# Kernel tuning notes

Hardware: AMD Instinct MI355X
Metric: run time of the kernel (lower is better)

## Reference

```python
import jax, jax.numpy as jnp
import numpy as np
from jax import lax

D_MODEL = 512
N_STATE = 64
L = 1024
NC = 4  # n_components
HIDDEN = 2 * D_MODEL  # ChannelMix mult=2
R = D_MODEL // 8      # SE reduction
EPS = 1e-5


def hippo_A(N):
    n = np.arange(N, dtype=np.float32)
    t = 2.0 * n + 1.0
    sq = np.sqrt(t[:, None] * t[None, :])
    A = -np.tril(sq, -1) - np.diag(n + 1.0)
    return jnp.asarray(A, jnp.float32)


def setup_inputs() -> dict:
    key = jax.random.key(0)
    ks = jax.random.split(key, 12)
    d, N = D_MODEL, N_STATE
    n = np.arange(N, dtype=np.float32)
    Bref = jnp.asarray(np.sqrt(2.0 * n + 1.0), jnp.float32)
    Bp = jnp.tile(Bref[None, None, :], (NC, d, 1)) + 0.01 * jax.random.normal(ks[0], (NC, d, N))
    Cp = 0.1 * jax.random.normal(ks[1], (NC, d, N))
    Dp = jnp.zeros((NC, d))
    log_dt = jnp.log(0.1 * (1.5 ** jnp.arange(NC, dtype=jnp.float32)))
    x = jax.random.normal(ks[2], (8, L, d))
    s = 0.02
    return {
        "x": x,
        "Bp": Bp, "Cp": Cp, "Dp": Dp, "log_dt": log_dt,
        "se_w1": s * jax.random.normal(ks[3], (R, d)), "se_b1": jnp.zeros((R,)),
        "se_w2": s * jax.random.normal(ks[4], (d, R)), "se_b2": jnp.zeros((d,)),
        "n1_g": jnp.ones((d,)), "n1_b": jnp.zeros((d,)),
        "up_w": s * jax.random.normal(ks[5], (2 * HIDDEN, d)), "up_b": jnp.zeros((2 * HIDDEN,)),
        "down_w": s * jax.random.normal(ks[6], (d, HIDDEN)), "down_b": jnp.zeros((d,)),
        "mixn_g": jnp.ones((d,)), "mixn_b": jnp.zeros((d,)),
        "n2_g": jnp.ones((d,)), "n2_b": jnp.zeros((d,)),
    }


def _ln(x, g, b):
    m = jnp.mean(x, axis=-1, keepdims=True)
    v = jnp.mean(jnp.square(x - m), axis=-1, keepdims=True)
    return (x - m) * lax.rsqrt(v + EPS) * g + b


def _mixture_kernel(Bp, Cp, Dp, log_dt):
    A = hippo_A(N_STATE)
    I = jnp.eye(N_STATE, dtype=jnp.float32)

    def one(Bc, Cc, Dc, ldt):
        dt = jax.nn.softplus(ldt) + 1e-6
        lhs = I - 0.5 * dt * A
        rhs = I + 0.5 * dt * A
        A_bar = jnp.linalg.solve(lhs, rhs)          # (N,N)
        B_bar = jnp.linalg.solve(lhs, (dt * Bc).T).T  # (d,N)

        def step(xs, _):
            y = jnp.einsum('dn,dn->d', Cc, xs)
            return xs @ A_bar.T, y

        _, ys = lax.scan(step, B_bar, None, length=L)  # (L,d)
        K = ys.T  # (d,L)
        return K.at[:, 0].add(Dc)

    return jax.vmap(one)(Bp, Cp, Dp, log_dt).sum(0)  # (d,L)


def reference(x, Bp, Cp, Dp, log_dt,
              se_w1, se_b1, se_w2, se_b2,
              n1_g, n1_b, up_w, up_b, down_w, down_b,
              mixn_g, mixn_b, n2_g, n2_b):
    d = D_MODEL
    K = _mixture_kernel(Bp, Cp, Dp, log_dt)  # (d,L)

    # causal full-length depthwise conv1d
    x_dw = jnp.transpose(x, (0, 2, 1))  # (B,C,T)
    x_pad = jnp.pad(x_dw, ((0, 0), (0, 0), (L - 1, 0)))
    y = lax.conv_general_dilated(
        x_pad, K[:, None, :], window_strides=(1,), padding='VALID',
        feature_group_count=d, dimension_numbers=('NCH', 'OIH', 'NCH'))
    y = jnp.transpose(y, (0, 2, 1))  # (B,T,C)

    # SE gate (squeeze over time)
    s = jnp.mean(y, axis=1)  # (B,C)
    h = jax.nn.relu(s @ se_w1.T + se_b1)
    g = jax.nn.sigmoid(h @ se_w2.T + se_b2)
    y = y * g[:, None, :]

    y1 = _ln(x + y, n1_g, n1_b)

    # ChannelMix (GLU MLP) with residual + LN
    u = y1 @ up_w.T + up_b
    a, gg = jnp.split(u, 2, axis=-1)
    z = (jax.nn.gelu(a, approximate=False) * jax.nn.sigmoid(gg)) @ down_w.T + down_b
    z = _ln(y1 + z, mixn_g, mixn_b)

    return _ln(y1 + z, n2_g, n2_b)
```

## Files before the change

### kernel.cpp

```cpp
#include <hip/hip_runtime.h>
#include <math.h>


typedef short bf16x8 __attribute__((ext_vector_type(8)));
typedef float f32x4 __attribute__((ext_vector_type(4)));

__device__ __forceinline__ float sigmoidf_(float x) { return 1.0f / (1.0f + expf(-x)); }
__device__ __forceinline__ float fast_sigmoid(float x) { return 1.0f / (1.0f + __expf(-x)); }
__device__ __forceinline__ float fast_gelu(float x) {
    float u = 0.7978845608f * (x + 0.044715f * x * x * x);
    float t = 1.0f - 2.0f / (1.0f + __expf(2.0f * u));
    return 0.5f * x * (1.0f + t);
}
__device__ __forceinline__ unsigned short f2bf(float f) {
    unsigned u = __float_as_uint(f);
    unsigned r = (u + 0x7FFFu + ((u >> 16) & 1u)) >> 16;
    return (unsigned short)r;
}
__device__ __forceinline__ unsigned pk2(unsigned short a, unsigned short b) {
    return (unsigned)a | ((unsigned)b << 16);
}
__device__ __forceinline__ void gload16(const void* g, void* l) {
    __builtin_amdgcn_global_load_lds((const __attribute__((address_space(1))) unsigned int*)g,
                                     (__attribute__((address_space(3))) unsigned int*)l, 16, 0, 0);
}

__global__ __launch_bounds__(256) void prep_comp(const float* __restrict__ log_dt,
                                                 float* __restrict__ Pow,
                                                 float* __restrict__ dtbuf) {
    int comp = blockIdx.x, tid = threadIdx.x;
    __shared__ __align__(16) float M1[4096];
    __shared__ __align__(16) float M1T[4096];
    __shared__ __align__(16) float M2[4096];
    __shared__ __align__(16) float M2T[4096];
    float ldt = log_dt[comp];
    float dt = log1pf(expf(ldt)) + 1e-6f;
    float hdt = 0.5f * dt;
    if (tid < 64) {
        int j = tid;
        float sqj = sqrtf(2.0f * (float)j + 1.0f);
        float S = 0.0f;
        for (int i = 0; i < 64; ++i) {
            float sqi = sqrtf(2.0f * (float)i + 1.0f);
            float r = (i == j) ? (1.0f - hdt * (float)(i + 1))
                               : ((i > j) ? (-hdt * sqi * sqj) : 0.0f);
            float X = (r - hdt * sqi * S) / (1.0f + hdt * (float)(i + 1));
            M1[i * 64 + j] = X;
            M1T[j * 64 + i] = X;
            S += sqi * X;
        }
    }
    __syncthreads();
    for (int ii = tid; ii < 4096; ii += 256) Pow[(size_t)comp * 40960 + ii] = M1[ii];
    float* cur = M1; float* curT = M1T; float* nxt = M2; float* nxtT = M2T;
    int ti = tid >> 4, tj = tid & 15;
    for (int s = 1; s <= 9; ++s) {
        float c[4][4] = {{0}};
#pragma unroll 8
        for (int k = 0; k < 64; ++k) {
            float4 a = *(const float4*)&curT[k * 64 + ti * 4];
            float4 b = *(const float4*)&cur[k * 64 + tj * 4];
            c[0][0] += a.x * b.x; c[0][1] += a.x * b.y; c[0][2] += a.x * b.z; c[0][3] += a.x * b.w;
            c[1][0] += a.y * b.x; c[1][1] += a.y * b.y; c[1][2] += a.y * b.z; c[1][3] += a.y * b.w;
            c[2][0] += a.z * b.x; c[2][1] += a.z * b.y; c[2][2] += a.z * b.z; c[2][3] += a.z * b.w;
            c[3][0] += a.w * b.x; c[3][1] += a.w * b.y; c[3][2] += a.w * b.z; c[3][3] += a.w * b.w;
        }
#pragma unroll
        for (int r = 0; r < 4; ++r) {
            float4 row; row.x = c[r][0]; row.y = c[r][1]; row.z = c[r][2]; row.w = c[r][3];
            *(float4*)&nxt[(ti * 4 + r) * 64 + tj * 4] = row;
            float4 colv; colv.x = c[0][r]; colv.y = c[1][r]; colv.z = c[2][r]; colv.w = c[3][r];
            *(float4*)&nxtT[(tj * 4 + r) * 64 + ti * 4] = colv;
        }
        __syncthreads();
        for (int ii = tid; ii < 4096; ii += 256) Pow[(size_t)comp * 40960 + s * 4096 + ii] = nxt[ii];
        float* t0 = cur; cur = nxt; nxt = t0;
        float* t1 = curT; curT = nxtT; nxtT = t1;
        __syncthreads();
    }
    if (tid == 0) dtbuf[comp] = dt;
}

__global__ __launch_bounds__(256) void compute_bbar(const float* __restrict__ Bp,
                                                    const float* __restrict__ dtbuf,
                                                    unsigned short* __restrict__ Bb_h,
                                                    unsigned short* __restrict__ Bb_l) {
    int gid = blockIdx.x * 256 + threadIdx.x;
    int comp = gid >> 9;
    float dt = dtbuf[comp];
    float hdt = 0.5f * dt;
    const float* bp = Bp + (size_t)gid * 64;
    unsigned short* oh = Bb_h + (size_t)gid * 64;
    unsigned short* ol = Bb_l + (size_t)gid * 64;
    float S = 0.0f;
    for (int i = 0; i < 64; ++i) {
        float sqi = sqrtf(2.0f * (float)i + 1.0f);
        float y = (dt * bp[i] - hdt * sqi * S) / (1.0f + hdt * (float)(i + 1));
        unsigned short h = f2bf(y);
        oh[i] = h;
        ol[i] = f2bf(y - __uint_as_float((unsigned)h << 16));
        S += sqi * y;
    }
}

__global__ __launch_bounds__(256) void convert_all(const float* __restrict__ up_w,
                                                   const float* __restrict__ dn_w,
                                                   const float* __restrict__ Cp,
                                                   unsigned short* __restrict__ up_wb,
                                                   unsigned short* __restrict__ dn_wb,
                                                   unsigned short* __restrict__ Cp_h,
                                                   unsigned short* __restrict__ Cp_l) {
    int i = blockIdx.x * 256 + threadIdx.x;
    if (i < 196608) {
        const float* src = (i < 131072) ? up_w : dn_w;
        unsigned short* dst = (i < 131072) ? up_wb : dn_wb;
        int j = (i < 131072) ? i : (i - 131072);
        float4 a = ((const float4*)src)[2 * j];
        float4 b = ((const float4*)src)[2 * j + 1];
        uint4 o;
        o.x = pk2(f2bf(a.x), f2bf(a.y));
        o.y = pk2(f2bf(a.z), f2bf(a.w));
        o.z = pk2(f2bf(b.x), f2bf(b.y));
        o.w = pk2(f2bf(b.z), f2bf(b.w));
        *(uint4*)&dst[(size_t)j * 8] = o;
    } else if (i < 212992) {
        int j = i - 196608;
        float4 a = ((const float4*)Cp)[2 * j];
        float4 b = ((const float4*)Cp)[2 * j + 1];
        float vv[8] = {a.x, a.y, a.z, a.w, b.x, b.y, b.z, b.w};
        unsigned short hs[8], ls[8];
#pragma unroll
        for (int k = 0; k < 8; ++k) {
            unsigned short h = f2bf(vv[k]);
            hs[k] = h;
            ls[k] = f2bf(vv[k] - __uint_as_float((unsigned)h << 16));
        }
        uint4 ho, lo;
        ho.x = pk2(hs[0], hs[1]); ho.y = pk2(hs[2], hs[3]); ho.z = pk2(hs[4], hs[5]); ho.w = pk2(hs[6], hs[7]);
        lo.x = pk2(ls[0], ls[1]); lo.y = pk2(ls[2], ls[3]); lo.z = pk2(ls[4], ls[5]); lo.w = pk2(ls[6], ls[7]);
        *(uint4*)&Cp_h[(size_t)j * 8] = ho;
        *(uint4*)&Cp_l[(size_t)j * 8] = lo;
    }
}

__global__ __launch_bounds__(256) void power_mats(const float* __restrict__ Pow,
                                                  unsigned short* __restrict__ Pst_h,
                                                  unsigned short* __restrict__ Pst_l,
                                                  unsigned short* __restrict__ Qst_h,
                                                  unsigned short* __restrict__ Qst_l) {
    int idx = blockIdx.x, comp = blockIdx.y, tid = threadIdx.x;
    __shared__ __align__(16) float R[4096], RT[4096], R2[4096], R2T[4096], SbT[4096];
    int isP = (idx < 32) ? 1 : 0;
    int f = isP ? idx : (idx - 32);
    int base_s = isP ? 0 : 5;
    const float* PowC = Pow + (size_t)comp * 40960;
    int i_ = tid & 63, kc = (tid >> 6) * 16;
    float* cur = R; float* curT = RT; float* nx = R2; float* nxT = R2T;
    if (f == 0) {
        for (int ii = tid; ii < 4096; ii += 256) {
            float v = ((ii >> 6) == (ii & 63)) ? 1.0f : 0.0f;
            R[ii] = v; RT[ii] = v;
        }
        __syncthreads();
    } else {
        int b0 = __ffs(f) - 1;
        const float* S0 = PowC + (size_t)(base_s + b0) * 4096;
#pragma unroll
        for (int j = 0; j < 16; j += 4) {
            float4 v = *(const float4*)&S0[i_ * 64 + kc + j];
            *(float4*)&R[i_ * 64 + kc + j] = v;
            RT[(kc + j + 0) * 64 + i_] = v.x;
            RT[(kc + j + 1) * 64 + i_] = v.y;
            RT[(kc + j + 2) * 64 + i_] = v.z;
            RT[(kc + j + 3) * 64 + i_] = v.w;
        }
        int rem = f & ~(1 << b0);
        int ti = tid >> 4, tj = tid & 15;
        __syncthreads();
        while (rem) {
            int b = __ffs(rem) - 1; rem &= rem - 1;
            const float* Sb = PowC + (size_t)(base_s + b) * 4096;
#pragma unroll
            for (int j = 0; j < 16; j += 4) {
                float4 v = *(const float4*)&Sb[i_ * 64 + kc + j];
                SbT[(kc + j + 0) * 64 + i_] = v.x;
                SbT[(kc + j + 1) * 64 + i_] = v.y;
                SbT[(kc + j + 2) * 64 + i_] = v.z;
                SbT[(kc + j + 3) * 64 + i_] = v.w;
            }
            __syncthreads();
            float c[4][4] = {{0}};
#pragma unroll 8
            for (int k = 0; k < 64; ++k) {
                float4 a = *(const float4*)&SbT[k * 64 + ti * 4];
                float4 b4 = *(const float4*)&cur[k * 64 + tj * 4];
                c[0][0] += a.x * b4.x; c[0][1] += a.x * b4.y; c[0][2] += a.x * b4.z; c[0][3] += a.x * b4.w;
                c[1][0] += a.y * b4.x; c[1][1] += a.y * b4.y; c[1][2] += a.y * b4.z; c[1][3] += a.y * b4.w;
                c[2][0] += a.z * b4.x; c[2][1] += a.z * b4.y; c[2][2] += a.z * b4.z; c[2][3] += a.z * b4.w;
                c[3][0] += a.w * b4.x; c[3][1] += a.w * b4.y; c[3][2] += a.w * b4.z; c[3][3] += a.w * b4.w;
            }
#pragma unroll
            for (int r = 0; r < 4; ++r) {
                float4 row; row.x = c[r][0]; row.y = c[r][1]; row.z = c[r][2]; row.w = c[r][3];
                *(float4*)&nx[(ti * 4 + r) * 64 + tj * 4] = row;
                float4 colv; colv.x = c[0][r]; colv.y = c[1][r]; colv.z = c[2][r]; colv.w = c[3][r];
                *(float4*)&nxT[(tj * 4 + r) * 64 + ti * 4] = colv;
            }
            __syncthreads();
            float* t0 = cur; cur = nx; nx = t0;
            float* t1 = curT; curT = nxT; nxT = t1;
        }
    }
    const float* src = isP ? cur : curT;
    int outrow = isP ? idx : (idx - 32);
    unsigned short* dh = (isP ? Pst_h : Qst_h) + (size_t)comp * 131072 + (size_t)outrow * 4096;
    unsigned short* dl = (isP ? Pst_l : Qst_l) + (size_t)comp * 131072 + (size_t)outrow * 4096;
    for (int ii = tid * 8; ii < 4096; ii += 2048) {
        float4 v0 = *(const float4*)&src[ii];
        float4 v1 = *(const float4*)&src[ii + 4];
        float vv[8] = {v0.x, v0.y, v0.z, v0.w, v1.x, v1.y, v1.z, v1.w};
        unsigned short hs[8], ls[8];
#pragma unroll
        for (int j = 0; j < 8; ++j) {
            unsigned short h = f2bf(vv[j]);
            hs[j] = h;
            ls[j] = f2bf(vv[j] - __uint_as_float((unsigned)h << 16));
        }
        uint4 ho, lo;
        ho.x = pk2(hs[0], hs[1]); ho.y = pk2(hs[2], hs[3]); ho.z = pk2(hs[4], hs[5]); ho.w = pk2(hs[6], hs[7]);
        lo.x = pk2(ls[0], ls[1]); lo.y = pk2(ls[2], ls[3]); lo.z = pk2(ls[4], ls[5]); lo.w = pk2(ls[6], ls[7]);
        *(uint4*)&dh[ii] = ho;
        *(uint4*)&dl[ii] = lo;
    }
}

__global__ __launch_bounds__(256) void kgemm_uv2(const unsigned short* __restrict__ Bb_h,
                                                 const unsigned short* __restrict__ Bb_l,
                                                 const unsigned short* __restrict__ Pst_h,
                                                 const unsigned short* __restrict__ Pst_l,
                                                 const unsigned short* __restrict__ Cp_h,
                                                 const unsigned short* __restrict__ Cp_l,
                                                 const unsigned short* __restrict__ Qst_h,
                                                 const unsigned short* __restrict__ Qst_l,
                                                 unsigned short* __restrict__ V_h,
                                                 unsigned short* __restrict__ V_l,
                                                 unsigned short* __restrict__ U_h,
                                                 unsigned short* __restrict__ U_l) {
    int zz = blockIdx.z;
    int isV = (zz < 4) ? 1 : 0;
    int comp = isV ? zz : (zz - 4);
    const unsigned short* Ah = isV ? Bb_h : Cp_h;
    const unsigned short* Al = isV ? Bb_l : Cp_l;
    const unsigned short* Bh = isV ? Pst_h : Qst_h;
    const unsigned short* Bl = isV ? Pst_l : Qst_l;
    unsigned short* Ch = isV ? V_h : U_h;
    unsigned short* Cl = isV ? V_l : U_l;
    int m0 = blockIdx.x * 128, n0 = blockIdx.y * 64;
    int tid = threadIdx.x, w = tid >> 6, l = tid & 63;
    __shared__ __align__(16) short Ash[8192], Asl[8192], Bsh[4096], Bsl[4096];
    const unsigned short* Abh = Ah + (size_t)comp * 32768;
    const unsigned short* Abl = Al + (size_t)comp * 32768;
    const unsigned short* Bbh = Bh + (size_t)comp * 131072;
    const unsigned short* Bbl = Bl + (size_t)comp * 131072;
#pragma unroll
    for (int i = 0; i < 4; ++i) {
        int cid = tid + 256 * i;
        int row = cid >> 3, slot = cid & 7;
        int goff = (m0 + row) * 64 + slot * 8;
        int loff = row * 64 + (slot ^ (row & 7)) * 8;
        *(uint4*)&Ash[loff] = *(const uint4*)(Abh + goff);
        *(uint4*)&Asl[loff] = *(const uint4*)(Abl + goff);
    }
#pragma unroll
    for (int i = 0; i < 2; ++i) {
        int cid = tid + 256 * i;
        int row = cid >> 3, slot = cid & 7;
        int goff = (n0 + row) * 64 + slot * 8;
        int loff = row * 64 + (slot ^ (row & 7)) * 8;
        *(uint4*)&Bsh[loff] = *(const uint4*)(Bbh + goff);
        *(uint4*)&Bsl[loff] = *(const uint4*)(Bbl + goff);
    }
    __syncthreads();
    int p = l >> 4, lr = l & 15;
    f32x4 acc[2][4];
#pragma unroll
    for (int rt = 0; rt < 2; ++rt)
#pragma unroll
        for (int ct = 0; ct < 4; ++ct) acc[rt][ct] = (f32x4)0.0f;
#pragma unroll
    for (int ks = 0; ks < 2; ++ks) {
        bf16x8 ah2[2], al2[2], bh2[4], bl2[4];
#pragma unroll
        for (int rt = 0; rt < 2; ++rt) {
            int row = w * 32 + rt * 16 + lr;
            int off = row * 64 + ((ks * 4 + p) ^ (row & 7)) * 8;
            ah2[rt] = *(bf16x8*)&Ash[off];
            al2[rt] = *(bf16x8*)&Asl[off];
        }
#pragma unroll
        for (int ct = 0; ct < 4; ++ct) {
            int cr = ct * 16 + lr;
            int off = cr * 64 + ((ks * 4 + p) ^ (cr & 7)) * 8;
            bh2[ct] = *(bf16x8*)&Bsh[off];
            bl2[ct] = *(bf16x8*)&Bsl[off];
        }
#pragma unroll
        for (int rt = 0; rt < 2; ++rt)
#pragma unroll
            for (int ct = 0; ct < 4; ++ct) {
                acc[rt][ct] = __builtin_amdgcn_mfma_f32_16x16x32_bf16(ah2[rt], bh2[ct], acc[rt][ct], 0, 0, 0);
                acc[rt][ct] = __builtin_amdgcn_mfma_f32_16x16x32_bf16(ah2[rt], bl2[ct], acc[rt][ct], 0, 0, 0);
                acc[rt][ct] = __builtin_amdgcn_mfma_f32_16x16x32_bf16(al2[rt], bh2[ct], acc[rt][ct], 0, 0, 0);
            }
    }
#pragma unroll
    for (int rt = 0; rt < 2; ++rt)
#pragma unroll
        for (int ct = 0; ct < 4; ++ct) {
#pragma unroll
            for (int reg = 0; reg < 4; ++reg) {
                int row = m0 + w * 32 + rt * 16 + p * 4 + reg;
                int col = n0 + ct * 16 + lr;
                float v = acc[rt][ct][reg];
                unsigned short h = f2bf(v);
                unsigned short lo2 = f2bf(v - __uint_as_float((unsigned)h << 16));
                size_t o = (size_t)comp * 1048576 + (size_t)row * 2048 + col;
                Ch[o] = h;
                Cl[o] = lo2;
            }
        }
}

__global__ __launch_bounds__(256) void kgemm_kr(const unsigned short* __restrict__ Uh,
                                                const unsigned short* __restrict__ Ul,
                                                const unsigned short* __restrict__ Vh,
                                                const unsigned short* __restrict__ Vl,
                                                const float* __restrict__ Dp,
                                                float* __restrict__ Kr) {
    int tid = threadIdx.x, w = tid >> 6, l = tid & 63;
    int d = blockIdx.x;
    int g = w * 512 + d;
    int p = l >> 4, lr = l & 15;
    __shared__ float ksh[4096];
    const unsigned short* ubh = Uh + (size_t)g * 2048;
    const unsigned short* ubl = Ul + (size_t)g * 2048;
    const unsigned short* vbh = Vh + (size_t)g * 2048;
    const unsigned short* vbl = Vl + (size_t)g * 2048;
    f32x4 acc[2][2];
    acc[0][0] = (f32x4)0.0f; acc[0][1] = (f32x4)0.0f;
    acc[1][0] = (f32x4)0.0f; acc[1][1] = (f32x4)0.0f;
#pragma unroll
    for (int ks = 0; ks < 2; ++ks) {
        bf16x8 uh2[2], ul2[2], vh2[2], vl2[2];
#pragma unroll
        for (int mt = 0; mt < 2; ++mt) {
            int off = (mt * 16 + lr) * 64 + ks * 32 + p * 8;
            uh2[mt] = *(const bf16x8*)(ubh + off);
            ul2[mt] = *(const bf16x8*)(ubl + off);
            vh2[mt] = *(const bf16x8*)(vbh + off);
            vl2[mt] = *(const bf16x8*)(vbl + off);
        }
#pragma unroll
        for (int mt = 0; mt < 2; ++mt)
#pragma unroll
            for (int nt = 0; nt < 2; ++nt) {
                acc[mt][nt] = __builtin_amdgcn_mfma_f32_16x16x32_bf16(uh2[mt], vh2[nt], acc[mt][nt], 0, 0, 0);
                acc[mt][nt] = __builtin_amdgcn_mfma_f32_16x16x32_bf16(uh2[mt], vl2[nt], acc[mt][nt], 0, 0, 0);
                acc[mt][nt] = __builtin_amdgcn_mfma_f32_16x16x32_bf16(ul2[mt], vh2[nt], acc[mt][nt], 0, 0, 0);
            }
    }
#pragma unroll
    for (int mt = 0; mt < 2; ++mt)
#pragma unroll
        for (int nt = 0; nt < 2; ++nt)
#pragma unroll
            for (int reg = 0; reg < 4; ++reg) {
                int q = mt * 16 + p * 4 + reg;
                int r = nt * 16 + lr;
                ksh[w * 1024 + q * 32 + r] = acc[mt][nt][reg];
            }
    __syncthreads();
#pragma unroll
    for (int j = 0; j < 4; ++j) {
        int ll = tid * 4 + j;
        float s = ksh[ll] + ksh[1024 + ll] + ksh[2048 + ll] + ksh[3072 + ll];
        if (ll == 0) s += Dp[d] + Dp[512 + d] + Dp[1024 + d] + Dp[1536 + d];
        Kr[(size_t)d * 1024 + (1023 - ll)] = s;
    }
}

__global__ __launch_bounds__(256) void transpose_bmat(const float* __restrict__ in,
                                                      float* __restrict__ out,
                                                      int R, int C) {
    __shared__ float tile[32][33];
    int r0 = blockIdx.x * 32, c0 = blockIdx.y * 32, b = blockIdx.z;
    int tx = threadIdx.x & 31, ty = threadIdx.x >> 5;
#pragma unroll
    for (int m = 0; m < 4; ++m)
        tile[ty + 8 * m][tx] = in[((size_t)b * R + r0 + ty + 8 * m) * C + c0 + tx];
    __syncthreads();
#pragma unroll
    for (int m = 0; m < 4; ++m)
        out[((size_t)b * C + c0 + ty + 8 * m) * R + r0 + tx] = tile[tx][ty + 8 * m];
}

__global__ __launch_bounds__(256) void conv_mfma(const float* __restrict__ xT,
                                                 const float* __restrict__ Kr,
                                                 float* __restrict__ yT,
                                                 float* __restrict__ ssum) {
    int c = blockIdx.x, tid = threadIdx.x;
    int w = tid >> 6, l = tid & 63;
    __shared__ __align__(16) float krp[1088];
    __shared__ __align__(16) short xh[8512], xl[8512];
    __shared__ __align__(16) short gh[10240], gl[10240];
    __shared__ float ssh[64];

    {
        float4 kv = *(const float4*)&Kr[(size_t)c * 1024 + tid * 4];
        *(float4*)&krp[32 + tid * 4] = kv;
        if (tid < 8) *(float4*)&krp[tid * 4] = make_float4(0, 0, 0, 0);
        else if (tid < 16) *(float4*)&krp[1056 + (tid - 8) * 4] = make_float4(0, 0, 0, 0);
    }
    if (tid < 32) {
        int b = tid >> 2, g = tid & 3;
        uint4 z = {0, 0, 0, 0};
        *(uint4*)&xh[(b * 133 + g) * 8] = z;
    } else if (tid < 64) {
        int t2 = tid - 32; int b = t2 >> 2, g = t2 & 3;
        uint4 z = {0, 0, 0, 0};
        *(uint4*)&xl[(b * 133 + g) * 8] = z;
    }
#pragma unroll
    for (int i = 0; i < 4; ++i) {
        int gid = tid + 256 * i;
        int b = gid >> 7, gt = gid & 127;
        const float* src = &xT[((size_t)(b * 512 + c)) * 1024 + gt * 8];
        float4 v0 = *(const float4*)src;
        float4 v1 = *(const float4*)(src + 4);
        float vv[8] = {v0.x, v0.y, v0.z, v0.w, v1.x, v1.y, v1.z, v1.w};
        unsigned short hsv[8], lsv[8];
#pragma unroll
        for (int j2 = 0; j2 < 8; ++j2) {
            unsigned short h = f2bf(vv[j2]);
            hsv[j2] = h;
            lsv[j2] = f2bf(vv[j2] - __uint_as_float((unsigned)h << 16));
        }
        uint4 hh, ll;
        hh.x = pk2(hsv[0], hsv[1]); hh.y = pk2(hsv[2], hsv[3]);
        hh.z = pk2(hsv[4], hsv[5]); hh.w = pk2(hsv[6], hsv[7]);
        ll.x = pk2(lsv[0], lsv[1]); ll.y = pk2(lsv[2], lsv[3]);
        ll.z = pk2(lsv[4], lsv[5]); ll.w = pk2(lsv[6], lsv[7]);
        int off = (b * 133 + 4 + gt) * 8;
        *(uint4*)&xh[off] = hh;
        *(uint4*)&xl[off] = ll;
    }
    __syncthreads();

    f32x4 acc[4][2];
#pragma unroll
    for (int i = 0; i < 4; ++i) { acc[i][0] = (f32x4)0.0f; acc[i][1] = (f32x4)0.0f; }

    int lr = l & 15, kg4 = l >> 4;
    for (int ch = 0; ch < 4; ++ch) {
        int dq0 = ch * 8;
        {
            int dqloc = tid >> 5, n = tid & 31, dq = dq0 + dqloc;
            int s0 = 32 * dq + n + 1;
            int a0 = s0 & ~3, sh = s0 & 3;
            float ff[36];
#pragma unroll
            for (int i = 0; i < 9; ++i) *(float4*)&ff[i * 4] = *(const float4*)&krp[a0 + i * 4];
            unsigned short hsv[32], lsv[32];
#pragma unroll
            for (int k = 0; k < 32; ++k) {
                int j2 = 31 - k;
                float v = (sh == 0) ? ff[j2] : (sh == 1) ? ff[j2 + 1] : (sh == 2) ? ff[j2 + 2] : ff[j2 + 3];
                unsigned short h = f2bf(v);
                hsv[k] = h;
                lsv[k] = f2bf(v - __uint_as_float((unsigned)h << 16));
            }
            int gbase = (dqloc * 32 + n) * 5 * 8;
#pragma unroll
            for (int kg = 0; kg < 4; ++kg) {
                uint4 hh, ll;
                hh.x = pk2(hsv[8 * kg + 0], hsv[8 * kg + 1]);
                hh.y = pk2(hsv[8 * kg + 2], hsv[8 * kg + 3]);
                hh.z = pk2(hsv[8 * kg + 4], hsv[8 * kg + 5]);
                hh.w = pk2(hsv[8 * kg + 6], hsv[8 * kg + 7]);
                ll.x = pk2(lsv[8 * kg + 0], lsv[8 * kg + 1]);
                ll.y = pk2(lsv[8 * kg + 2], lsv[8 * kg + 3]);
                ll.z = pk2(lsv[8 * kg + 4], lsv[8 * kg + 5]);
                ll.w = pk2(lsv[8 * kg + 6], lsv[8 * kg + 7]);
                *(uint4*)&gh[gbase + kg * 8] = hh;
                *(uint4*)&gl[gbase + kg * 8] = ll;
            }
        }
        __syncthreads();
        for (int dqloc = 0; dqloc < 8; ++dqloc) {
            int dq = dq0 + dqloc;
            bf16x8 bh[2], bl[2];
#pragma unroll
            for (int nf = 0; nf < 2; ++nf) {
                int go = ((dqloc * 32 + nf * 16 + lr) * 5 + kg4) * 8;
                bh[nf] = *(bf16x8*)&gh[go];
                bl[nf] = *(bf16x8*)&gl[go];
            }
#pragma unroll
            for (int ffi = 0; ffi < 4; ++ffi) {
                int F = w + 4 * ffi;
                if (2 * F + 1 < dq) continue;
                int b = lr & 7, qoff = lr >> 3;
                int q = 2 * F + qoff;
                int j = 4 * (q - dq) + kg4 + 4;
                int xo = (b * 133 + j) * 8;
                bf16x8 ah = *(bf16x8*)&xh[xo];
                bf16x8 al = *(bf16x8*)&xl[xo];
#pragma unroll
                for (int nf = 0; nf < 2; ++nf) {
                    acc[ffi][nf] = __builtin_amdgcn_mfma_f32_16x16x32_bf16(ah, bh[nf], acc[ffi][nf], 0, 0, 0);
                    acc[ffi][nf] = __builtin_amdgcn_mfma_f32_16x16x32_bf16(al, bh[nf], acc[ffi][nf], 0, 0, 0);
                    acc[ffi][nf] = __builtin_amdgcn_mfma_f32_16x16x32_bf16(ah, bl[nf], acc[ffi][nf], 0, 0, 0);
                }
            }
        }
        __syncthreads();
    }

    float bsum[4] = {0, 0, 0, 0};
#pragma unroll
    for (int ffi = 0; ffi < 4; ++ffi) {
        int F = w + 4 * ffi;
#pragma unroll
        for (int nf = 0; nf < 2; ++nf) {
#pragma unroll
            for (int reg = 0; reg < 4; ++reg) {
                int mloc = 4 * kg4 + reg;
                int b = mloc & 7;
                int q = 2 * F + (mloc >> 3);
                int t = 32 * q + nf * 16 + lr;
                yT[((size_t)(b * 512 + c)) * 1024 + t] = acc[ffi][nf][reg];
                bsum[reg] += acc[ffi][nf][reg];
            }
        }
    }
#pragma unroll
    for (int off = 1; off < 16; off <<= 1) {
#pragma unroll
        for (int reg = 0; reg < 4; ++reg) bsum[reg] += __shfl_xor(bsum[reg], off, 64);
    }
    if (lr == 0) {
#pragma unroll
        for (int reg = 0; reg < 4; ++reg) ssh[w * 16 + kg4 * 4 + reg] = bsum[reg];
    }
    __syncthreads();
    if (tid < 8) {
        float tot = 0.0f;
        for (int w2 = 0; w2 < 4; ++w2) tot += ssh[w2 * 16 + tid] + ssh[w2 * 16 + 8 + tid];
        ssum[tid * 512 + c] = tot;
    }
}

__global__ __launch_bounds__(256) void se_kernel(const float* __restrict__ ssum,
                                                 const float* __restrict__ w1,
                                                 const float* __restrict__ b1,
                                                 const float* __restrict__ w2,
                                                 const float* __restrict__ b2,
                                                 float* __restrict__ g) {
    int b = blockIdx.x, tid = threadIdx.x;
    __shared__ float s_sh[512];
    __shared__ float part[256];
    __shared__ float h_sh[64];
    for (int c = tid; c < 512; c += 256) s_sh[c] = ssum[b * 512 + c] * (1.0f / 1024.0f);
    __syncthreads();
    int r = tid & 63, seg = tid >> 6;
    float p = 0.0f;
    for (int c = seg * 128; c < seg * 128 + 128; ++c) p += s_sh[c] * w1[r * 512 + c];
    part[tid] = p;
    __syncthreads();
    if (tid < 64) {
        float h = part[tid] + part[tid + 64] + part[tid + 128] + part[tid + 192] + b1[tid];
        h_sh[tid] = fmaxf(h, 0.0f);
    }
    __syncthreads();
    for (int c = tid; c < 512; c += 256) {
        float acc = b2[c];
#pragma unroll 8
        for (int rr = 0; rr < 64; ++rr) acc += h_sh[rr] * w2[c * 64 + rr];
        g[b * 512 + c] = 1.0f / (1.0f + expf(-acc));
    }
}

__global__ __launch_bounds__(128) void fuse1_kernel(const float* __restrict__ x,
                                                    const float* __restrict__ y,
                                                    const float* __restrict__ g,
                                                    const float* __restrict__ n1g,
                                                    const float* __restrict__ n1b,
                                                    unsigned short* __restrict__ y1b) {
    int row = blockIdx.x, b = row >> 10, tid = threadIdx.x, c = tid * 4;
    __shared__ float r1[2], r2[2];
    float4 xv = *(const float4*)&x[(size_t)row * 512 + c];
    float4 yv = *(const float4*)&y[(size_t)row * 512 + c];
    float4 gv = *(const float4*)&g[b * 512 + c];
    float4 v;
    v.x = xv.x + yv.x * gv.x; v.y = xv.y + yv.y * gv.y;
    v.z = xv.z + yv.z * gv.z; v.w = xv.w + yv.w * gv.w;
    float s1 = v.x + v.y + v.z + v.w;
    float s2 = v.x * v.x + v.y * v.y + v.z * v.z + v.w * v.w;
#pragma unroll
    for (int off = 32; off > 0; off >>= 1) {
        s1 += __shfl_down(s1, off, 64);
        s2 += __shfl_down(s2, off, 64);
    }
    if ((tid & 63) == 0) { r1[tid >> 6] = s1; r2[tid >> 6] = s2; }
    __syncthreads();
    float mean = (r1[0] + r1[1]) * (1.0f / 512.0f);
    float var = (r2[0] + r2[1]) * (1.0f / 512.0f) - mean * mean;
    float rstd = rsqrtf(var + 1e-5f);
    float4 g4 = *(const float4*)&n1g[c];
    float4 b4 = *(const float4*)&n1b[c];
    float4 o;
    o.x = (v.x - mean) * rstd * g4.x + b4.x; o.y = (v.y - mean) * rstd * g4.y + b4.y;
    o.z = (v.z - mean) * rstd * g4.z + b4.z; o.w = (v.w - mean) * rstd * g4.w + b4.w;
    uint2 pk;
    pk.x = pk2(f2bf(o.x), f2bf(o.y));
    pk.y = pk2(f2bf(o.z), f2bf(o.w));
    *(uint2*)&y1b[(size_t)row * 512 + c] = pk;
}

__device__ __forceinline__ int swz_slot(int slot, int row) {
    return slot ^ (row & 3) ^ ((row >> 2) & 3);
}

__global__ __launch_bounds__(256) void gemm_glu(const unsigned short* __restrict__ A,
                                                const unsigned short* __restrict__ W,
                                                const float* __restrict__ bias,
                                                unsigned short* __restrict__ act) {
    const int K = 512;
    int id = blockIdx.x;
    int xcd = id & 7, local = id >> 3;
    int bx = 16 * xcd + (local & 15);
    int by = local >> 4;
    int m0 = bx * 64, n0 = by * 64;
    int tid = threadIdx.x, w = tid >> 6, l = tid & 63;
    __shared__ __align__(16) short As[2][2048];
    __shared__ __align__(16) short Bs[2][4096];
    int rA = w * 16 + (l >> 2);
    int sA = (l & 3) ^ (rA & 3) ^ ((rA >> 2) & 3);
    const unsigned short* gA = A + (size_t)(m0 + rA) * K + sA * 8;
    int rB0 = w * 32 + (l >> 2);
    int rB1 = w * 32 + 16 + (l >> 2);
    int sB0 = (l & 3) ^ (rB0 & 3) ^ ((rB0 >> 2) & 3);
    int sB1 = (l & 3) ^ (rB1 & 3) ^ ((rB1 >> 2) & 3);
    int gRow0 = (rB0 < 64) ? (n0 + rB0) : (1024 + n0 + rB0 - 64);
    int gRow1 = (rB1 < 64) ? (n0 + rB1) : (1024 + n0 + rB1 - 64);
    const unsigned short* gB0 = W + (size_t)gRow0 * K + sB0 * 8;
    const unsigned short* gB1 = W + (size_t)gRow1 * K + sB1 * 8;
    int p = l >> 4, lr = l & 15;
    int aoff;
    { int r = w * 16 + lr; aoff = r * 32 + swz_slot(p, r) * 8; }
    int bAoff[4], bGoff[4];
#pragma unroll
    for (int ct = 0; ct < 4; ++ct) {
        int ca = ct * 16 + lr, cg = 64 + ct * 16 + lr;
        bAoff[ct] = ca * 32 + swz_slot(p, ca) * 8;
        bGoff[ct] = cg * 32 + swz_slot(p, cg) * 8;
    }
    f32x4 accA[4], accG[4];
#pragma unroll
    for (int ct = 0; ct < 4; ++ct) { accA[ct] = (f32x4)0.0f; accG[ct] = (f32x4)0.0f; }
    gload16(gA, &As[0][w * 512]);
    gload16(gB0, &Bs[0][w * 1024]);
    gload16(gB1, &Bs[0][w * 1024 + 512]);
    int cur = 0;
    for (int kt = 0; kt < K; kt += 32) {
        __syncthreads();
        if (kt + 32 < K) {
            int nb = cur ^ 1;
            gload16(gA + kt + 32, &As[nb][w * 512]);
            gload16(gB0 + kt + 32, &Bs[nb][w * 1024]);
            gload16(gB1 + kt + 32, &Bs[nb][w * 1024 + 512]);
        }
        bf16x8 af = *(bf16x8*)&As[cur][aoff];
        bf16x8 bA[4], bG[4];
#pragma unroll
        for (int ct = 0; ct < 4; ++ct) {
            bA[ct] = *(bf16x8*)&Bs[cur][bAoff[ct]];
            bG[ct] = *(bf16x8*)&Bs[cur][bGoff[ct]];
        }
#pragma unroll
        for (int ct = 0; ct < 4; ++ct) {
            accA[ct] = __builtin_amdgcn_mfma_f32_16x16x32_bf16(af, bA[ct], accA[ct], 0, 0, 0);
            accG[ct] = __builtin_amdgcn_mfma_f32_16x16x32_bf16(af, bG[ct], accG[ct], 0, 0, 0);
        }
        cur ^= 1;
    }
#pragma unroll
    for (int ct = 0; ct < 4; ++ct) {
        int col = n0 + ct * 16 + lr;
        float ba = bias[col], bg = bias[1024 + col];
#pragma unroll
        for (int reg = 0; reg < 4; ++reg) {
            int row = m0 + w * 16 + p * 4 + reg;
            float a = accA[ct][reg] + ba;
            float g = accG[ct][reg] + bg;
            act[(size_t)row * 1024 + col] = f2bf(fast_gelu(a) * fast_sigmoid(g));
        }
    }
}

__global__ __launch_bounds__(256) void gemm_plain(const unsigned short* __restrict__ A,
                                                  const unsigned short* __restrict__ W,
                                                  const float* __restrict__ bias,
                                                  float* __restrict__ Cout) {
    const int K = 1024, N = 512;
    int id = blockIdx.x;
    int xcd = id & 7, local = id >> 3;
    int bx = 16 * xcd + (local & 15);
    int by = local >> 4;
    int m0 = bx * 64, n0 = by * 64;
    int tid = threadIdx.x, w = tid >> 6, l = tid & 63;
    int wr = w >> 1, wc = w & 1;
    __shared__ __align__(16) short As[2][2048];
    __shared__ __align__(16) short Bs[2][2048];
    int rA = w * 16 + (l >> 2);
    int sA = (l & 3) ^ (rA & 3) ^ ((rA >> 2) & 3);
    const unsigned short* gA = A + (size_t)(m0 + rA) * K + sA * 8;
    const unsigned short* gB = W + (size_t)(n0 + rA) * K + sA * 8;
    int p = l >> 4, lr = l & 15;
    int aoff[2], boff[2];
#pragma unroll
    for (int t = 0; t < 2; ++t) {
        int r = wr * 32 + t * 16 + lr;
        aoff[t] = r * 32 + swz_slot(p, r) * 8;
        int cq = wc * 32 + t * 16 + lr;
        boff[t] = cq * 32 + swz_slot(p, cq) * 8;
    }
    f32x4 acc[2][2];
#pragma unroll
    for (int i = 0; i < 2; ++i)
#pragma unroll
        for (int j = 0; j < 2; ++j) acc[i][j] = (f32x4)0.0f;
    gload16(gA, &As[0][w * 512]);
    gload16(gB, &Bs[0][w * 512]);
    int cur = 0;
    for (int kt = 0; kt < K; kt += 32) {
        __syncthreads();
        if (kt + 32 < K) {
            int nb = cur ^ 1;
            gload16(gA + kt + 32, &As[nb][w * 512]);
            gload16(gB + kt + 32, &Bs[nb][w * 512]);
        }
        bf16x8 af[2], bfr[2];
#pragma unroll
        for (int t = 0; t < 2; ++t) {
            af[t] = *(bf16x8*)&As[cur][aoff[t]];
            bfr[t] = *(bf16x8*)&Bs[cur][boff[t]];
        }
#pragma unroll
        for (int i = 0; i < 2; ++i)
#pragma unroll
            for (int j = 0; j < 2; ++j)
                acc[i][j] = __builtin_amdgcn_mfma_f32_16x16x32_bf16(af[i], bfr[j], acc[i][j], 0, 0, 0);
        cur ^= 1;
    }
#pragma unroll
    for (int i = 0; i < 2; ++i)
#pragma unroll
        for (int j = 0; j < 2; ++j) {
            int col = n0 + wc * 32 + j * 16 + lr;
            float bb = bias[col];
#pragma unroll
            for (int reg = 0; reg < 4; ++reg) {
                int row = m0 + wr * 32 + i * 16 + p * 4 + reg;
                Cout[(size_t)row * N + col] = acc[i][j][reg] + bb;
            }
        }
}

__global__ __launch_bounds__(128) void fuse2_kernel(const unsigned short* __restrict__ y1b,
                                                    const float* __restrict__ z,
                                                    const float* __restrict__ mg,
                                                    const float* __restrict__ mb,
                                                    const float* __restrict__ g2,
                                                    const float* __restrict__ b2v,
                                                    float* __restrict__ out) {
    int row = blockIdx.x, tid = threadIdx.x, c = tid * 4;
    __shared__ float r1[2], r2[2];
    uint2 yu = *(const uint2*)&y1b[(size_t)row * 512 + c];
    float4 a;
    a.x = __uint_as_float(yu.x << 16);
    a.y = __uint_as_float(yu.x & 0xffff0000u);
    a.z = __uint_as_float(yu.y << 16);
    a.w = __uint_as_float(yu.y & 0xffff0000u);
    float4 zv = *(const float4*)&z[(size_t)row * 512 + c];
    float4 t1;
    t1.x = a.x + zv.x; t1.y = a.y + zv.y; t1.z = a.z + zv.z; t1.w = a.w + zv.w;
    float s1 = t1.x + t1.y + t1.z + t1.w;
    float s2 = t1.x * t1.x + t1.y * t1.y + t1.z * t1.z + t1.w * t1.w;
#pragma unroll
    for (int off = 32; off > 0; off >>= 1) {
        s1 += __shfl_down(s1, off, 64);
        s2 += __shfl_down(s2, off, 64);
    }
    if ((tid & 63) == 0) { r1[tid >> 6] = s1; r2[tid >> 6] = s2; }
    __syncthreads();
    float mean = (r1[0] + r1[1]) * (1.0f / 512.0f);
    float var = (r2[0] + r2[1]) * (1.0f / 512.0f) - mean * mean;
    float rstd = rsqrtf(var + 1e-5f);
    float4 mg4 = *(const float4*)&mg[c];
    float4 mb4 = *(const float4*)&mb[c];
    float4 t2;
    t2.x = a.x + ((t1.x - mean) * rstd * mg4.x + mb4.x);
    t2.y = a.y + ((t1.y - mean) * rstd * mg4.y + mb4.y);
    t2.z = a.z + ((t1.z - mean) * rstd * mg4.z + mb4.z);
    t2.w = a.w + ((t1.w - mean) * rstd * mg4.w + mb4.w);
    __syncthreads();
    s1 = t2.x + t2.y + t2.z + t2.w;
    s2 = t2.x * t2.x + t2.y * t2.y + t2.z * t2.z + t2.w * t2.w;
#pragma unroll
    for (int off = 32; off > 0; off >>= 1) {
        s1 += __shfl_down(s1, off, 64);
        s2 += __shfl_down(s2, off, 64);
    }
    if ((tid & 63) == 0) { r1[tid >> 6] = s1; r2[tid >> 6] = s2; }
    __syncthreads();
    float mean2 = (r1[0] + r1[1]) * (1.0f / 512.0f);
    float var2 = (r2[0] + r2[1]) * (1.0f / 512.0f) - mean2 * mean2;
    float rstd2 = rsqrtf(var2 + 1e-5f);
    float4 gg = *(const float4*)&g2[c];
    float4 bb = *(const float4*)&b2v[c];
    float4 o;
    o.x = (t2.x - mean2) * rstd2 * gg.x + bb.x;
    o.y = (t2.y - mean2) * rstd2 * gg.y + bb.y;
    o.z = (t2.z - mean2) * rstd2 * gg.z + bb.z;
    o.w = (t2.w - mean2) * rstd2 * gg.w + bb.w;
    *(float4*)&out[(size_t)row * 512 + c] = o;
}

extern "C" void kernel_launch(void* const* d_in, const int* in_sizes, int n_in,
                              void* d_out, int out_size, void* d_ws, size_t ws_size,
                              hipStream_t stream) {
    (void)in_sizes; (void)n_in; (void)out_size; (void)ws_size;
    const float* x      = (const float*)d_in[0];
    const float* Bp     = (const float*)d_in[1];
    const float* Cp     = (const float*)d_in[2];
    const float* Dp     = (const float*)d_in[3];
    const float* log_dt = (const float*)d_in[4];
    const float* se_w1  = (const float*)d_in[5];
    const float* se_b1  = (const float*)d_in[6];
    const float* se_w2  = (const float*)d_in[7];
    const float* se_b2  = (const float*)d_in[8];
    const float* n1g    = (const float*)d_in[9];
    const float* n1b    = (const float*)d_in[10];
    const float* up_w   = (const float*)d_in[11];
    const float* up_b   = (const float*)d_in[12];
    const float* dn_w   = (const float*)d_in[13];
    const float* dn_b   = (const float*)d_in[14];
    const float* mxg    = (const float*)d_in[15];
    const float* mxb    = (const float*)d_in[16];
    const float* n2g    = (const float*)d_in[17];
    const float* n2b    = (const float*)d_in[18];

    float* ws = (float*)d_ws;
    float* Kr   = ws + 0;
    float* dtb  = ws + 524288;
    float* ssum = ws + 524352;
    float* gbuf = ws + 528448;
    unsigned short* up_wb = (unsigned short*)(ws + 532544);
    unsigned short* dn_wb = (unsigned short*)(ws + 1056832);
    float* Pow  = ws + 1450048;
    unsigned short* Bb_h = (unsigned short*)(ws + 1613888);
    unsigned short* Bb_l = (unsigned short*)(ws + 1679424);
    unsigned short* Cp_h = (unsigned short*)(ws + 1744960);
    unsigned short* Cp_l = (unsigned short*)(ws + 1810496);
    unsigned short* Pst_h = (unsigned short*)(ws + 1876032);
    unsigned short* Pst_l = (unsigned short*)(ws + 2138176);
    unsigned short* Qst_h = (unsigned short*)(ws + 2400320);
    unsigned short* Qst_l = (unsigned short*)(ws + 2662464);
    unsigned short* U_h = (unsigned short*)(ws + 5021760);
    unsigned short* U_l = (unsigned short*)(ws + 7118912);
    unsigned short* V_h = (unsigned short*)(ws + 9216064);
    unsigned short* V_l = (unsigned short*)(ws + 11313216);
    float* xT   = ws + 5021760;
    float* yT   = ws + 9216064;
    float* yb   = ws + 13410368;
    unsigned short* y1b = (unsigned short*)(ws + 9216064);
    unsigned short* act = (unsigned short*)(ws + 5021760);
    float* zb   = ws + 13410368;
    float* outp = (float*)d_out;

    hipLaunchKernelGGL(prep_comp, dim3(4), dim3(256), 0, stream, log_dt, Pow, dtb);
    hipLaunchKernelGGL(compute_bbar, dim3(8), dim3(256), 0, stream, Bp, dtb, Bb_h, Bb_l);
    hipLaunchKernelGGL(convert_all, dim3(832), dim3(256), 0, stream, up_w, dn_w, Cp, up_wb, dn_wb, Cp_h, Cp_l);
    hipLaunchKernelGGL(power_mats, dim3(64, 4), dim3(256), 0, stream, Pow, Pst_h, Pst_l, Qst_h, Qst_l);
    hipLaunchKernelGGL(kgemm_uv2, dim3(4, 32, 8), dim3(256), 0, stream,
                       Bb_h, Bb_l, Pst_h, Pst_l, Cp_h, Cp_l, Qst_h, Qst_l, V_h, V_l, U_h, U_l);
    hipLaunchKernelGGL(kgemm_kr, dim3(512), dim3(256), 0, stream, U_h, U_l, V_h, V_l, Dp, Kr);
    hipLaunchKernelGGL(transpose_bmat, dim3(32, 16, 8), dim3(256), 0, stream, x, xT, 1024, 512);
    hipLaunchKernelGGL(conv_mfma, dim3(512), dim3(256), 0, stream, xT, Kr, yT, ssum);
    hipLaunchKernelGGL(se_kernel, dim3(8), dim3(256), 0, stream, ssum, se_w1, se_b1, se_w2, se_b2, gbuf);
    hipLaunchKernelGGL(transpose_bmat, dim3(16, 32, 8), dim3(256), 0, stream, yT, yb, 512, 1024);
    hipLaunchKernelGGL(fuse1_kernel, dim3(8192), dim3(128), 0, stream, x, yb, gbuf, n1g, n1b, y1b);
    hipLaunchKernelGGL(gemm_glu, dim3(2048), dim3(256), 0, stream, y1b, up_wb, up_b, act);
    hipLaunchKernelGGL(gemm_plain, dim3(1024), dim3(256), 0, stream, act, dn_wb, dn_b, zb);
    hipLaunchKernelGGL(fuse2_kernel, dim3(8192), dim3(128), 0, stream, y1b, zb, mxg, mxb, n2g, n2b, outp);
}
```

Before: 239.7 us.

## Fuse y transpose into LayerNorm kernel and deepen GEMM K-tiles to 64

Drops the separate transpose of the conv output. A new fused kernel reads the time-major yT directly through a padded shared-memory tile, then applies the SE gate, residual and LayerNorm for 16 timesteps per block. Both MLP GEMMs now stage 64-wide K slices with an 8-way XOR swizzle, so the loop runs half as many iterations and barriers. The cost is more LDS per block, which may lower occupancy. The y1b buffer moves to a new workspace offset, which needs a large enough workspace.

```diff
diff --git a/kernel.cpp b/kernel.cpp
--- a/kernel.cpp
+++ b/kernel.cpp
@@ -590,46 +590,71 @@
     }
 }
 
-__global__ __launch_bounds__(128) void fuse1_kernel(const float* __restrict__ x,
-                                                    const float* __restrict__ y,
-                                                    const float* __restrict__ g,
-                                                    const float* __restrict__ n1g,
-                                                    const float* __restrict__ n1b,
-                                                    unsigned short* __restrict__ y1b) {
-    int row = blockIdx.x, b = row >> 10, tid = threadIdx.x, c = tid * 4;
-    __shared__ float r1[2], r2[2];
-    float4 xv = *(const float4*)&x[(size_t)row * 512 + c];
-    float4 yv = *(const float4*)&y[(size_t)row * 512 + c];
-    float4 gv = *(const float4*)&g[b * 512 + c];
-    float4 v;
-    v.x = xv.x + yv.x * gv.x; v.y = xv.y + yv.y * gv.y;
-    v.z = xv.z + yv.z * gv.z; v.w = xv.w + yv.w * gv.w;
-    float s1 = v.x + v.y + v.z + v.w;
-    float s2 = v.x * v.x + v.y * v.y + v.z * v.z + v.w * v.w;
-#pragma unroll
-    for (int off = 32; off > 0; off >>= 1) {
-        s1 += __shfl_down(s1, off, 64);
-        s2 += __shfl_down(s2, off, 64);
-    }
-    if ((tid & 63) == 0) { r1[tid >> 6] = s1; r2[tid >> 6] = s2; }
-    __syncthreads();
-    float mean = (r1[0] + r1[1]) * (1.0f / 512.0f);
-    float var = (r2[0] + r2[1]) * (1.0f / 512.0f) - mean * mean;
+__global__ __launch_bounds__(256) void fuse1t(const float* __restrict__ x,
+                                              const float* __restrict__ yT,
+                                              const float* __restrict__ g,
+                                              const float* __restrict__ n1g,
+                                              const float* __restrict__ n1b,
+                                              unsigned short* __restrict__ y1b) {
+    int ti = blockIdx.x, b = blockIdx.y, t0 = ti * 16, tid = threadIdx.x;
+    __shared__ float tile[512 * 17];
+    __shared__ float red1[256], red2[256];
+    for (int i = tid; i < 2048; i += 256) {
+        int c = i >> 2, tq = (i & 3) * 4;
+        float4 v = *(const float4*)&yT[((size_t)(b * 512 + c)) * 1024 + t0 + tq];
+        tile[c * 17 + tq + 0] = v.x;
+        tile[c * 17 + tq + 1] = v.y;
+        tile[c * 17 + tq + 2] = v.z;
+        tile[c * 17 + tq + 3] = v.w;
+    }
+    __syncthreads();
+    int tloc = tid >> 4, cg = tid & 15;
+    int t = t0 + tloc;
+    float vbuf[32];
+    float s1 = 0.0f, s2 = 0.0f;
+#pragma unroll
+    for (int m = 0; m < 8; ++m) {
+        int c = cg * 4 + 64 * m;
+        float4 xv = *(const float4*)&x[((size_t)(b * 1024 + t)) * 512 + c];
+        float4 gv = *(const float4*)&g[b * 512 + c];
+        float v0 = xv.x + tile[(c + 0) * 17 + tloc] * gv.x;
+        float v1 = xv.y + tile[(c + 1) * 17 + tloc] * gv.y;
+        float v2 = xv.z + tile[(c + 2) * 17 + tloc] * gv.z;
+        float v3 = xv.w + tile[(c + 3) * 17 + tloc] * gv.w;
+        vbuf[m * 4 + 0] = v0; vbuf[m * 4 + 1] = v1;
+        vbuf[m * 4 + 2] = v2; vbuf[m * 4 + 3] = v3;
+        s1 += v0 + v1 + v2 + v3;
+        s2 += v0 * v0 + v1 * v1 + v2 * v2 + v3 * v3;
+    }
+    red1[tid] = s1; red2[tid] = s2;
+    __syncthreads();
+    if (cg == 0) {
+        float a1 = 0.0f, a2 = 0.0f;
+#pragma unroll
+        for (int k = 0; k < 16; ++k) { a1 += red1[tloc * 16 + k]; a2 += red2[tloc * 16 + k]; }
+        red1[tloc * 16] = a1; red2[tloc * 16] = a2;
+    }
+    __syncthreads();
+    float mean = red1[tloc * 16] * (1.0f / 512.0f);
+    float var = red2[tloc * 16] * (1.0f / 512.0f) - mean * mean;
     float rstd = rsqrtf(var + 1e-5f);
-    float4 g4 = *(const float4*)&n1g[c];
-    float4 b4 = *(const float4*)&n1b[c];
-    float4 o;
-    o.x = (v.x - mean) * rstd * g4.x + b4.x; o.y = (v.y - mean) * rstd * g4.y + b4.y;
-    o.z = (v.z - mean) * rstd * g4.z + b4.z; o.w = (v.w - mean) * rstd * g4.w + b4.w;
-    uint2 pk;
-    pk.x = pk2(f2bf(o.x), f2bf(o.y));
-    pk.y = pk2(f2bf(o.z), f2bf(o.w));
-    *(uint2*)&y1b[(size_t)row * 512 + c] = pk;
-}
-
-__device__ __forceinline__ int swz_slot(int slot, int row) {
-    return slot ^ (row & 3) ^ ((row >> 2) & 3);
-}
+#pragma unroll
+    for (int m = 0; m < 8; ++m) {
+        int c = cg * 4 + 64 * m;
+        float4 g4 = *(const float4*)&n1g[c];
+        float4 b4 = *(const float4*)&n1b[c];
+        float o0 = (vbuf[m * 4 + 0] - mean) * rstd * g4.x + b4.x;
+        float o1 = (vbuf[m * 4 + 1] - mean) * rstd * g4.y + b4.y;
+        float o2 = (vbuf[m * 4 + 2] - mean) * rstd * g4.z + b4.z;
+        float o3 = (vbuf[m * 4 + 3] - mean) * rstd * g4.w + b4.w;
+        uint2 pk;
+        pk.x = pk2(f2bf(o0), f2bf(o1));
+        pk.y = pk2(f2bf(o2), f2bf(o3));
+        *(uint2*)&y1b[((size_t)(b * 1024 + t)) * 512 + c] = pk;
+    }
+}
+
+__device__ __forceinline__ int swz8(int slot, int row) { return slot ^ (row & 7); }
 
 __global__ __launch_bounds__(256) void gemm_glu(const unsigned short* __restrict__ A,
                                                 const unsigned short* __restrict__ W,
@@ -642,55 +667,58 @@
     int by = local >> 4;
     int m0 = bx * 64, n0 = by * 64;
     int tid = threadIdx.x, w = tid >> 6, l = tid & 63;
-    __shared__ __align__(16) short As[2][2048];
-    __shared__ __align__(16) short Bs[2][4096];
-    int rA = w * 16 + (l >> 2);
-    int sA = (l & 3) ^ (rA & 3) ^ ((rA >> 2) & 3);
-    const unsigned short* gA = A + (size_t)(m0 + rA) * K + sA * 8;
-    int rB0 = w * 32 + (l >> 2);
-    int rB1 = w * 32 + 16 + (l >> 2);
-    int sB0 = (l & 3) ^ (rB0 & 3) ^ ((rB0 >> 2) & 3);
-    int sB1 = (l & 3) ^ (rB1 & 3) ^ ((rB1 >> 2) & 3);
-    int gRow0 = (rB0 < 64) ? (n0 + rB0) : (1024 + n0 + rB0 - 64);
-    int gRow1 = (rB1 < 64) ? (n0 + rB1) : (1024 + n0 + rB1 - 64);
-    const unsigned short* gB0 = W + (size_t)gRow0 * K + sB0 * 8;
-    const unsigned short* gB1 = W + (size_t)gRow1 * K + sB1 * 8;
+    __shared__ __align__(16) short As[2][4096];
+    __shared__ __align__(16) short Bs[2][8192];
+    const unsigned short* gA[2];
+#pragma unroll
+    for (int i = 0; i < 2; ++i) {
+        int s = 2 * w + i;
+        int row = 8 * s + (l >> 3);
+        gA[i] = A + (size_t)(m0 + row) * K + (size_t)(((l & 7) ^ (row & 7)) * 8);
+    }
+    const unsigned short* gB[4];
+#pragma unroll
+    for (int i = 0; i < 4; ++i) {
+        int s = 4 * w + i;
+        int rb = 8 * s + (l >> 3);
+        int grow = (rb < 64) ? (n0 + rb) : (1024 + n0 + rb - 64);
+        gB[i] = W + (size_t)grow * K + (size_t)(((l & 7) ^ (rb & 7)) * 8);
+    }
     int p = l >> 4, lr = l & 15;
-    int aoff;
-    { int r = w * 16 + lr; aoff = r * 32 + swz_slot(p, r) * 8; }
-    int bAoff[4], bGoff[4];
-#pragma unroll
-    for (int ct = 0; ct < 4; ++ct) {
-        int ca = ct * 16 + lr, cg = 64 + ct * 16 + lr;
-        bAoff[ct] = ca * 32 + swz_slot(p, ca) * 8;
-        bGoff[ct] = cg * 32 + swz_slot(p, cg) * 8;
-    }
+    int arow = w * 16 + lr;
     f32x4 accA[4], accG[4];
 #pragma unroll
     for (int ct = 0; ct < 4; ++ct) { accA[ct] = (f32x4)0.0f; accG[ct] = (f32x4)0.0f; }
-    gload16(gA, &As[0][w * 512]);
-    gload16(gB0, &Bs[0][w * 1024]);
-    gload16(gB1, &Bs[0][w * 1024 + 512]);
+#pragma unroll
+    for (int i = 0; i < 2; ++i) gload16(gA[i], &As[0][(2 * w + i) * 512]);
+#pragma unroll
+    for (int i = 0; i < 4; ++i) gload16(gB[i], &Bs[0][(4 * w + i) * 512]);
     int cur = 0;
-    for (int kt = 0; kt < K; kt += 32) {
+    for (int kt = 0; kt < K; kt += 64) {
         __syncthreads();
-        if (kt + 32 < K) {
+        if (kt + 64 < K) {
             int nb = cur ^ 1;
-            gload16(gA + kt + 32, &As[nb][w * 512]);
-            gload16(gB0 + kt + 32, &Bs[nb][w * 1024]);
-            gload16(gB1 + kt + 32, &Bs[nb][w * 1024 + 512]);
-        }
-        bf16x8 af = *(bf16x8*)&As[cur][aoff];
-        bf16x8 bA[4], bG[4];
-#pragma unroll
-        for (int ct = 0; ct < 4; ++ct) {
-            bA[ct] = *(bf16x8*)&Bs[cur][bAoff[ct]];
-            bG[ct] = *(bf16x8*)&Bs[cur][bGoff[ct]];
-        }
-#pragma unroll
-        for (int ct = 0; ct < 4; ++ct) {
-            accA[ct] = __builtin_amdgcn_mfma_f32_16x16x32_bf16(af, bA[ct], accA[ct], 0, 0, 0);
-            accG[ct] = __builtin_amdgcn_mfma_f32_16x16x32_bf16(af, bG[ct], accG[ct], 0, 0, 0);
+#pragma unroll
+            for (int i = 0; i < 2; ++i) gload16(gA[i] + kt + 64, &As[nb][(2 * w + i) * 512]);
+#pragma unroll
+            for (int i = 0; i < 4; ++i) gload16(gB[i] + kt + 64, &Bs[nb][(4 * w + i) * 512]);
+        }
+#pragma unroll
+        for (int ks = 0; ks < 2; ++ks) {
+            int slot = ks * 4 + p;
+            bf16x8 af = *(bf16x8*)&As[cur][arow * 64 + swz8(slot, arow) * 8];
+            bf16x8 bA[4], bG[4];
+#pragma unroll
+            for (int ct = 0; ct < 4; ++ct) {
+                int ca = ct * 16 + lr, cg = 64 + ct * 16 + lr;
+                bA[ct] = *(bf16x8*)&Bs[cur][ca * 64 + swz8(slot, ca) * 8];
+                bG[ct] = *(bf16x8*)&Bs[cur][cg * 64 + swz8(slot, cg) * 8];
+            }
+#pragma unroll
+            for (int ct = 0; ct < 4; ++ct) {
+                accA[ct] = __builtin_amdgcn_mfma_f32_16x16x32_bf16(af, bA[ct], accA[ct], 0, 0, 0);
+                accG[ct] = __builtin_amdgcn_mfma_f32_16x16x32_bf16(af, bG[ct], accG[ct], 0, 0, 0);
+            }
         }
         cur ^= 1;
     }
@@ -702,8 +730,8 @@
         for (int reg = 0; reg < 4; ++reg) {
             int row = m0 + w * 16 + p * 4 + reg;
             float a = accA[ct][reg] + ba;
-            float g = accG[ct][reg] + bg;
-            act[(size_t)row * 1024 + col] = f2bf(fast_gelu(a) * fast_sigmoid(g));
+            float gg = accG[ct][reg] + bg;
+            act[(size_t)row * 1024 + col] = f2bf(fast_gelu(a) * fast_sigmoid(gg));
         }
     }
 }
@@ -720,47 +748,57 @@
     int m0 = bx * 64, n0 = by * 64;
     int tid = threadIdx.x, w = tid >> 6, l = tid & 63;
     int wr = w >> 1, wc = w & 1;
-    __shared__ __align__(16) short As[2][2048];
-    __shared__ __align__(16) short Bs[2][2048];
-    int rA = w * 16 + (l >> 2);
-    int sA = (l & 3) ^ (rA & 3) ^ ((rA >> 2) & 3);
-    const unsigned short* gA = A + (size_t)(m0 + rA) * K + sA * 8;
-    const unsigned short* gB = W + (size_t)(n0 + rA) * K + sA * 8;
+    __shared__ __align__(16) short As[2][4096];
+    __shared__ __align__(16) short Bs[2][4096];
+    const unsigned short* gA[2];
+    const unsigned short* gB[2];
+#pragma unroll
+    for (int i = 0; i < 2; ++i) {
+        int s = 2 * w + i;
+        int row = 8 * s + (l >> 3);
+        int koff = ((l & 7) ^ (row & 7)) * 8;
+        gA[i] = A + (size_t)(m0 + row) * K + koff;
+        gB[i] = W + (size_t)(n0 + row) * K + koff;
+    }
     int p = l >> 4, lr = l & 15;
-    int aoff[2], boff[2];
-#pragma unroll
-    for (int t = 0; t < 2; ++t) {
-        int r = wr * 32 + t * 16 + lr;
-        aoff[t] = r * 32 + swz_slot(p, r) * 8;
-        int cq = wc * 32 + t * 16 + lr;
-        boff[t] = cq * 32 + swz_slot(p, cq) * 8;
-    }
     f32x4 acc[2][2];
 #pragma unroll
     for (int i = 0; i < 2; ++i)
 #pragma unroll
         for (int j = 0; j < 2; ++j) acc[i][j] = (f32x4)0.0f;
-    gload16(gA, &As[0][w * 512]);
-    gload16(gB, &Bs[0][w * 512]);
+#pragma unroll
+    for (int i = 0; i < 2; ++i) {
+        gload16(gA[i], &As[0][(2 * w + i) * 512]);
+        gload16(gB[i], &Bs[0][(2 * w + i) * 512]);
+    }
     int cur = 0;
-    for (int kt = 0; kt < K; kt += 32) {
+    for (int kt = 0; kt < K; kt += 64) {
         __syncthreads();
-        if (kt + 32 < K) {
+        if (kt + 64 < K) {
             int nb = cur ^ 1;
-            gload16(gA + kt + 32, &As[nb][w * 512]);
-            gload16(gB + kt + 32, &Bs[nb][w * 512]);
-        }
-        bf16x8 af[2], bfr[2];
-#pragma unroll
-        for (int t = 0; t < 2; ++t) {
-            af[t] = *(bf16x8*)&As[cur][aoff[t]];
-            bfr[t] = *(bf16x8*)&Bs[cur][boff[t]];
-        }
-#pragma unroll
-        for (int i = 0; i < 2; ++i)
-#pragma unroll
-            for (int j = 0; j < 2; ++j)
-                acc[i][j] = __builtin_amdgcn_mfma_f32_16x16x32_bf16(af[i], bfr[j], acc[i][j], 0, 0, 0);
+#pragma unroll
+            for (int i = 0; i < 2; ++i) {
+                gload16(gA[i] + kt + 64, &As[nb][(2 * w + i) * 512]);
+                gload16(gB[i] + kt + 64, &Bs[nb][(2 * w + i) * 512]);
+            }
+        }
+#pragma unroll
+        for (int ks = 0; ks < 2; ++ks) {
+            int slot = ks * 4 + p;
+            bf16x8 af[2], bfr[2];
+#pragma unroll
+            for (int t = 0; t < 2; ++t) {
+                int r = wr * 32 + t * 16 + lr;
+                af[t] = *(bf16x8*)&As[cur][r * 64 + swz8(slot, r) * 8];
+                int cq = wc * 32 + t * 16 + lr;
+                bfr[t] = *(bf16x8*)&Bs[cur][cq * 64 + swz8(slot, cq) * 8];
+            }
+#pragma unroll
+            for (int i = 0; i < 2; ++i)
+#pragma unroll
+                for (int j = 0; j < 2; ++j)
+                    acc[i][j] = __builtin_amdgcn_mfma_f32_16x16x32_bf16(af[i], bfr[j], acc[i][j], 0, 0, 0);
+        }
         cur ^= 1;
     }
 #pragma unroll
@@ -883,10 +921,9 @@
     unsigned short* V_l = (unsigned short*)(ws + 11313216);
     float* xT   = ws + 5021760;
     float* yT   = ws + 9216064;
-    float* yb   = ws + 13410368;
-    unsigned short* y1b = (unsigned short*)(ws + 9216064);
+    float* zb   = ws + 13410368;
     unsigned short* act = (unsigned short*)(ws + 5021760);
-    float* zb   = ws + 13410368;
+    unsigned short* y1b = (unsigned short*)(ws + 20971520);
     float* outp = (float*)d_out;
 
     hipLaunchKernelGGL(prep_comp, dim3(4), dim3(256), 0, stream, log_dt, Pow, dtb);
@@ -899,8 +936,7 @@
     hipLaunchKernelGGL(transpose_bmat, dim3(32, 16, 8), dim3(256), 0, stream, x, xT, 1024, 512);
     hipLaunchKernelGGL(conv_mfma, dim3(512), dim3(256), 0, stream, xT, Kr, yT, ssum);
     hipLaunchKernelGGL(se_kernel, dim3(8), dim3(256), 0, stream, ssum, se_w1, se_b1, se_w2, se_b2, gbuf);
-    hipLaunchKernelGGL(transpose_bmat, dim3(16, 32, 8), dim3(256), 0, stream, yT, yb, 512, 1024);
-    hipLaunchKernelGGL(fuse1_kernel, dim3(8192), dim3(128), 0, stream, x, yb, gbuf, n1g, n1b, y1b);
+    hipLaunchKernelGGL(fuse1t, dim3(64, 8), dim3(256), 0, stream, x, yT, gbuf, n1g, n1b, y1b);
     hipLaunchKernelGGL(gemm_glu, dim3(2048), dim3(256), 0, stream, y1b, up_wb, up_b, act);
     hipLaunchKernelGGL(gemm_plain, dim3(1024), dim3(256), 0, stream, act, dn_wb, dn_b, zb);
     hipLaunchKernelGGL(fuse2_kernel, dim3(8192), dim3(128), 0, stream, y1b, zb, mxg, mxb, n2g, n2b, outp);
```

Result: faster. 231.3 us (-3.5%).
